# Kernel optimization log

Measured on AMD Instinct MI355X. Metric: run time of the kernel, lower is better.

## Reference

```python
import jax, jax.numpy as jnp
import numpy as np
import math

N = 50000
E = 800000
C_IN = 32
C_H = 256
C_OUT = 3
DEPTH = 3
RATIO = 0.5


def setup_inputs() -> dict:
    key = jax.random.key(0)
    ks = jax.random.split(key, 16)
    s = 0.05  # keep tanh/relu in a healthy range
    f32 = jnp.float32
    return {
        "x": jax.random.normal(ks[0], (N, C_IN), f32),
        "edge_index": jax.random.randint(ks[1], (2, E), 0, N, jnp.int32).astype(jnp.int64),
        "w0_l": jax.random.normal(ks[2], (C_IN, C_H), f32) * s,
        "w0_r": jax.random.normal(ks[3], (C_IN, C_H), f32) * s,
        "b0": jax.random.normal(ks[4], (C_H,), f32) * s,
        "dwl": jax.random.normal(ks[5], (DEPTH, C_H, C_H), f32) * s,
        "dwr": jax.random.normal(ks[6], (DEPTH, C_H, C_H), f32) * s,
        "db": jax.random.normal(ks[7], (DEPTH, C_H), f32) * s,
        "pool_w": jax.random.normal(ks[8], (DEPTH, C_H), f32),
        "uwl": jax.random.normal(ks[9], (DEPTH - 1, C_H, C_H), f32) * s,
        "uwr": jax.random.normal(ks[10], (DEPTH - 1, C_H, C_H), f32) * s,
        "ub": jax.random.normal(ks[11], (DEPTH - 1, C_H), f32) * s,
        "uwl_last": jax.random.normal(ks[12], (C_H, C_OUT), f32) * s,
        "uwr_last": jax.random.normal(ks[13], (C_H, C_OUT), f32) * s,
        "ub_last": jax.random.normal(ks[14], (C_OUT,), f32) * s,
    }


def _sage_max(x, src, dst, n, wl, wr, b):
    # SAGEConv(aggr='max'): out = lin_l(max_j x_j) + lin_r(x_i)
    # dst may contain dummy index n (masked edges); slice it off.
    msg = x[src]                                            # [E, C]
    agg = jax.ops.segment_max(msg, dst, num_segments=n + 1)[:n]
    agg = jnp.where(jnp.isfinite(agg), agg, 0.0)            # empty segments -> 0 (PyG)
    return agg @ wl + b + x @ wr


def _topk_pool(x, src, dst, w, ratio):
    # PyG TopKPooling with min_score=None: score=tanh((x.w)/||w||), keep top-k, rescale.
    n = x.shape[0]
    k = math.ceil(ratio * n)
    score = jnp.tanh((x @ w) / jnp.linalg.norm(w))          # [n]
    vals, perm = jax.lax.top_k(score, k)
    x2 = x[perm] * vals[:, None]
    # relabel edges; dropped edges -> dummy node k (fixed shape, equivalent for max-agg)
    mapping = jnp.full((n + 1,), -1, jnp.int32).at[perm].set(jnp.arange(k, dtype=jnp.int32))
    nsrc, ndst = mapping[src], mapping[dst]
    valid = (nsrc >= 0) & (ndst >= 0)
    src2 = jnp.where(valid, nsrc, 0)
    dst2 = jnp.where(valid, ndst, k)
    return x2, src2, dst2, perm, k


def reference(x, edge_index, w0_l, w0_r, b0, dwl, dwr, db, pool_w,
              uwl, uwr, ub, uwl_last, uwr_last, ub_last):
    n = x.shape[0]
    src = edge_index[0].astype(jnp.int32)
    dst = edge_index[1].astype(jnp.int32)

    x = jax.nn.relu(_sage_max(x, src, dst, n, w0_l, w0_r, b0))
    xs, srcs, dsts, ns, perms = [x], [src], [dst], [n], []

    for i in range(DEPTH):
        x, src, dst, perm, n = _topk_pool(x, src, dst, pool_w[i], RATIO)
        x = jax.nn.relu(_sage_max(x, src, dst, n, dwl[i], dwr[i], db[i]))
        if i < DEPTH - 1:
            xs.append(x); srcs.append(src); dsts.append(dst); ns.append(n)
        perms.append(perm)

    for i in range(DEPTH):
        j = DEPTH - 1 - i
        res, src, dst, n, perm = xs[j], srcs[j], dsts[j], ns[j], perms[j]
        up = jnp.zeros_like(res).at[perm].set(x)
        x = res + up                                         # sum_res=True
        if i < DEPTH - 1:
            x = jax.nn.relu(_sage_max(x, src, dst, n, uwl[i], uwr[i], ub[i]))
        else:
            x = _sage_max(x, src, dst, n, uwl_last, uwr_last, ub_last)

    return jnp.tanh(x) * 0.5
```

## Files before the change

kernel.cpp:

```cpp
#include <hip/hip_runtime.h>
#include <math.h>

#define E_NUM 800000
#define CH 256

typedef __attribute__((ext_vector_type(8))) short short8;
typedef __attribute__((ext_vector_type(4))) float float4v;

__device__ __forceinline__ unsigned f2key(float s) {
  unsigned b = __float_as_uint(s);
  return (b & 0x80000000u) ? ~b : (b | 0x80000000u);
}

__device__ __forceinline__ unsigned pkmax_u16(unsigned a, unsigned b) {
  unsigned d;
  asm("v_pk_max_u16 %0, %1, %2" : "=v"(d) : "v"(a), "v"(b));
  return d;
}


__global__ __launch_bounds__(256) void k_deg(const int* __restrict__ dst, int n,
                                             int* __restrict__ deg) {
  int e = blockIdx.x * 256 + threadIdx.x;
  if (e < E_NUM) { int d = dst[e]; if (d < n) atomicAdd(&deg[d], 1); }
}

__global__ __launch_bounds__(256) void k_scan_block(const int* __restrict__ deg, int n,
                                                    int* __restrict__ incl,
                                                    int* __restrict__ bsum) {
  __shared__ int s[256];
  int i = blockIdx.x * 256 + threadIdx.x;
  int v = (i < n) ? deg[i] : 0;
  s[threadIdx.x] = v;
  __syncthreads();
  for (int o = 1; o < 256; o <<= 1) {
    int t = (threadIdx.x >= o) ? s[threadIdx.x - o] : 0;
    __syncthreads();
    s[threadIdx.x] += t;
    __syncthreads();
  }
  if (i < n) incl[i] = s[threadIdx.x];
  if (threadIdx.x == 255) bsum[blockIdx.x] = s[255];
}

__global__ void k_scan_bsum(int* bsum, int nb, int* total_out) {
  if (threadIdx.x == 0 && blockIdx.x == 0) {
    int acc = 0;
    for (int b = 0; b < nb; b++) { int v = bsum[b]; bsum[b] = acc; acc += v; }
    total_out[0] = acc;
  }
}

__global__ __launch_bounds__(256) void k_scan_final(const int* __restrict__ deg,
                                                    const int* __restrict__ incl,
                                                    const int* __restrict__ bsum, int n,
                                                    int* __restrict__ row,
                                                    int* __restrict__ cursor) {
  int i = blockIdx.x * 256 + threadIdx.x;
  if (i < n) {
    int r = incl[i] - deg[i] + bsum[blockIdx.x];
    row[i] = r;
    cursor[i] = r;
  }
}

__global__ __launch_bounds__(256) void k_fill(const int* __restrict__ src,
                                              const int* __restrict__ dst, int n,
                                              int* __restrict__ cursor,
                                              int* __restrict__ col) {
  int e = blockIdx.x * 256 + threadIdx.x;
  if (e < E_NUM) {
    int d = dst[e];
    if (d < n) { int p = atomicAdd(&cursor[d], 1); col[p] = src[e]; }
  }
}

__global__ __launch_bounds__(256) void k_relabel_deg(const int* __restrict__ srcIn,
                                                     const int* __restrict__ dstIn,
                                                     const int* __restrict__ mapping,
                                                     int kNew, int* __restrict__ srcOut,
                                                     int* __restrict__ dstOut,
                                                     int* __restrict__ deg) {
  int e = blockIdx.x * 256 + threadIdx.x;
  if (e >= E_NUM) return;
  int ns = mapping[srcIn[e]];
  int nd = mapping[dstIn[e]];
  if (ns >= 0 && nd >= 0) {
    srcOut[e] = ns;
    dstOut[e] = nd;
    atomicAdd(&deg[nd], 1);
  } else {
    srcOut[e] = 0;
    dstOut[e] = kNew;
  }
}


__device__ __forceinline__ float4 fmax4(float4 a, float4 b) {
  return make_float4(fmaxf(a.x, b.x), fmaxf(a.y, b.y), fmaxf(a.z, b.z), fmaxf(a.w, b.w));
}

__global__ __launch_bounds__(256) void k_aggmax32(const float* __restrict__ x,
                                                  const int* __restrict__ row,
                                                  const int* __restrict__ col,
                                                  float* __restrict__ out, int n) {
  int node = blockIdx.x * 8 + threadIdx.x / 32;
  int c = threadIdx.x % 32;
  if (node >= n) return;
  int e0 = row[node], e1 = row[node + 1];
  float m0 = -INFINITY, m1 = -INFINITY, m2 = -INFINITY, m3 = -INFINITY;
  int e = e0;
  for (; e + 4 <= e1; e += 4) {
    int s0 = col[e], s1 = col[e + 1], s2 = col[e + 2], s3 = col[e + 3];
    float v0 = x[(size_t)s0 * 32 + c];
    float v1 = x[(size_t)s1 * 32 + c];
    float v2 = x[(size_t)s2 * 32 + c];
    float v3 = x[(size_t)s3 * 32 + c];
    m0 = fmaxf(m0, v0); m1 = fmaxf(m1, v1); m2 = fmaxf(m2, v2); m3 = fmaxf(m3, v3);
  }
  for (; e < e1; e++) m0 = fmaxf(m0, x[(size_t)col[e] * 32 + c]);
  float m = fmaxf(fmaxf(m0, m1), fmaxf(m2, m3));
  out[(size_t)node * 32 + c] = (e1 > e0) ? m : 0.0f;
}

__global__ __launch_bounds__(256) void k_aggmax4(const float* __restrict__ x,
                                                 const int* __restrict__ row,
                                                 const int* __restrict__ col,
                                                 float* __restrict__ out, int n) {
  int lane = threadIdx.x & 63;
  int node = blockIdx.x * 4 + (threadIdx.x >> 6);
  if (node >= n) return;
  int e0 = row[node], e1 = row[node + 1];
  float4 m0 = make_float4(-INFINITY, -INFINITY, -INFINITY, -INFINITY);
  float4 m1 = m0, m2 = m0, m3 = m0;
  int e = e0;
  for (; e + 4 <= e1; e += 4) {
    int s0 = col[e], s1 = col[e + 1], s2 = col[e + 2], s3 = col[e + 3];
    float4 v0 = *(const float4*)&x[(size_t)s0 * CH + lane * 4];
    float4 v1 = *(const float4*)&x[(size_t)s1 * CH + lane * 4];
    float4 v2 = *(const float4*)&x[(size_t)s2 * CH + lane * 4];
    float4 v3 = *(const float4*)&x[(size_t)s3 * CH + lane * 4];
    m0 = fmax4(m0, v0); m1 = fmax4(m1, v1); m2 = fmax4(m2, v2); m3 = fmax4(m3, v3);
  }
  for (; e < e1; e++)
    m0 = fmax4(m0, *(const float4*)&x[(size_t)col[e] * CH + lane * 4]);
  float4 m = fmax4(fmax4(m0, m1), fmax4(m2, m3));
  if (e1 <= e0) m = make_float4(0.f, 0.f, 0.f, 0.f);
  *(float4*)&out[(size_t)node * CH + lane * 4] = m;
}

__device__ __forceinline__ float b2f(unsigned short s) {
  return __uint_as_float(((unsigned)s) << 16);
}

__global__ __launch_bounds__(256) void k_aggmax4_b16(const unsigned short* __restrict__ xb,
                                                     const int* __restrict__ row,
                                                     const int* __restrict__ col,
                                                     float* __restrict__ out, int n) {
  int lane = threadIdx.x & 63;
  int node = blockIdx.x * 4 + (threadIdx.x >> 6);
  if (node >= n) return;
  int e0 = row[node], e1 = row[node + 1];
  uint2 m0 = make_uint2(0u, 0u), m1 = m0, m2 = m0, m3 = m0;
  int e = e0;
  for (; e + 4 <= e1; e += 4) {
    int s0 = col[e], s1 = col[e + 1], s2 = col[e + 2], s3 = col[e + 3];
    uint2 v0 = *(const uint2*)&xb[(size_t)s0 * CH + lane * 4];
    uint2 v1 = *(const uint2*)&xb[(size_t)s1 * CH + lane * 4];
    uint2 v2 = *(const uint2*)&xb[(size_t)s2 * CH + lane * 4];
    uint2 v3 = *(const uint2*)&xb[(size_t)s3 * CH + lane * 4];
    m0.x = pkmax_u16(m0.x, v0.x); m0.y = pkmax_u16(m0.y, v0.y);
    m1.x = pkmax_u16(m1.x, v1.x); m1.y = pkmax_u16(m1.y, v1.y);
    m2.x = pkmax_u16(m2.x, v2.x); m2.y = pkmax_u16(m2.y, v2.y);
    m3.x = pkmax_u16(m3.x, v3.x); m3.y = pkmax_u16(m3.y, v3.y);
  }
  for (; e < e1; e++) {
    uint2 v = *(const uint2*)&xb[(size_t)col[e] * CH + lane * 4];
    m0.x = pkmax_u16(m0.x, v.x);
    m0.y = pkmax_u16(m0.y, v.y);
  }
  m0.x = pkmax_u16(pkmax_u16(m0.x, m1.x), pkmax_u16(m2.x, m3.x));
  m0.y = pkmax_u16(pkmax_u16(m0.y, m1.y), pkmax_u16(m2.y, m3.y));
  float4 m;
  m.x = b2f((unsigned short)(m0.x & 0xFFFFu));
  m.y = b2f((unsigned short)(m0.x >> 16));
  m.z = b2f((unsigned short)(m0.y & 0xFFFFu));
  m.w = b2f((unsigned short)(m0.y >> 16));
  *(float4*)&out[(size_t)node * CH + lane * 4] = m;
}


__global__ __launch_bounds__(256) void k_wprep(const float* __restrict__ src,
                                               unsigned short* __restrict__ dst, int K,
                                               int nmat) {
  int idx = blockIdx.x * 256 + threadIdx.x;
  int total = nmat * K * 256;
  if (idx >= total) return;
  int n = idx % 256;
  int k = (idx / 256) % K;
  int m = idx / (256 * K);
  float v = src[idx];
  unsigned u = __float_as_uint(v);
  unsigned h = u & 0xFFFF0000u;
  float r = v - __uint_as_float(h);
  unsigned short hs = (unsigned short)(h >> 16);
  unsigned short ls = (unsigned short)(__float_as_uint(r) >> 16);
  int ib = k >> 5, kk = k & 31;
  size_t base = (size_t)m * 2 * K * 256;
  size_t o = ((size_t)ib * 256 + n) * 32 + kk;
  dst[base + o] = hs;
  dst[base + (size_t)K * 256 + o] = ls;
}


#define KSTR 40

__global__ __launch_bounds__(256) void k_gemm_mfma(
    const float* __restrict__ A1, const float* __restrict__ A2,
    const unsigned short* __restrict__ W1t, const unsigned short* __restrict__ W2t,
    const float* __restrict__ bias, float* __restrict__ out, int M, int K, int scatter,
    const int* __restrict__ perm, const float* __restrict__ scw,
    float* __restrict__ score, unsigned* __restrict__ hist1) {
  __shared__ unsigned short As_h[64 * KSTR], As_l[64 * KSTR];
  __shared__ float sred[4][64];
  const int t = threadIdx.x;
  const int wave = t >> 6, lane = t & 63;
  const int l15 = lane & 15, qd = lane >> 4;
  const int bm0 = blockIdx.x * 64;
  float4v acc[4][4];
#pragma unroll
  for (int a = 0; a < 4; a++)
#pragma unroll
    for (int b = 0; b < 4; b++) acc[a][b] = (float4v)0.f;
  const int sa_m = t >> 2;
  const int sa_kc = (t & 3) * 8;
  const int rok = (bm0 + sa_m) < M;
  const int nIb = K >> 5;
  for (int ib = 0; ib < 2 * nIb; ib++) {
    const float* A = (ib < nIb) ? A1 : A2;
    const unsigned short* Wt = (ib < nIb) ? W1t : W2t;
    int ib0 = (ib < nIb) ? ib : ib - nIb;
    float va[8];
    {
      const float* ap = &A[(size_t)(bm0 + sa_m) * K + (ib0 << 5) + sa_kc];
      float4 v0 = rok ? *(const float4*)ap : make_float4(0, 0, 0, 0);
      float4 v1 = rok ? *(const float4*)(ap + 4) : make_float4(0, 0, 0, 0);
      va[0] = v0.x; va[1] = v0.y; va[2] = v0.z; va[3] = v0.w;
      va[4] = v1.x; va[5] = v1.y; va[6] = v1.z; va[7] = v1.w;
    }
    short8 bh[4], bl[4];
#pragma unroll
    for (int nt = 0; nt < 4; nt++) {
      size_t rowb = ((size_t)ib0 * 256 + wave * 64 + nt * 16 + l15) * 32 + qd * 8;
      bh[nt] = *(const short8*)&Wt[rowb];
      bl[nt] = *(const short8*)&Wt[(size_t)K * 256 + rowb];
    }
    unsigned hp[4], lp[4];
#pragma unroll
    for (int e = 0; e < 4; e++) {
      unsigned u0 = __float_as_uint(va[2 * e]);
      unsigned u1 = __float_as_uint(va[2 * e + 1]);
      unsigned h0 = u0 & 0xFFFF0000u, h1 = u1 & 0xFFFF0000u;
      float r0 = va[2 * e] - __uint_as_float(h0);
      float r1 = va[2 * e + 1] - __uint_as_float(h1);
      hp[e] = (h0 >> 16) | h1;
      lp[e] = (__float_as_uint(r0) >> 16) | (__float_as_uint(r1) & 0xFFFF0000u);
    }
    __syncthreads();
    *(uint4*)&As_h[sa_m * KSTR + sa_kc] = make_uint4(hp[0], hp[1], hp[2], hp[3]);
    *(uint4*)&As_l[sa_m * KSTR + sa_kc] = make_uint4(lp[0], lp[1], lp[2], lp[3]);
    __syncthreads();
    short8 ah[4], al[4];
#pragma unroll
    for (int mt = 0; mt < 4; mt++) {
      int r = (mt * 16 + l15) * KSTR + qd * 8;
      ah[mt] = *(const short8*)&As_h[r];
      al[mt] = *(const short8*)&As_l[r];
    }
#pragma unroll
    for (int mt = 0; mt < 4; mt++)
#pragma unroll
      for (int nt = 0; nt < 4; nt++) {
        acc[mt][nt] =
            __builtin_amdgcn_mfma_f32_16x16x32_bf16(bh[nt], ah[mt], acc[mt][nt], 0, 0, 0);
        acc[mt][nt] =
            __builtin_amdgcn_mfma_f32_16x16x32_bf16(bl[nt], ah[mt], acc[mt][nt], 0, 0, 0);
        acc[mt][nt] =
            __builtin_amdgcn_mfma_f32_16x16x32_bf16(bh[nt], al[mt], acc[mt][nt], 0, 0, 0);
      }
  }
  const int col0 = wave * 64;
  if (scw) {
    if (t < 64) { sred[0][t] = 0.f; sred[1][t] = 0.f; sred[2][t] = 0.f; sred[3][t] = 0.f; }
    __syncthreads();
  }
  float bias4[4][4], scw4[4][4];
#pragma unroll
  for (int nt = 0; nt < 4; nt++) {
    int cb = col0 + nt * 16 + qd * 4;
    *(float4*)bias4[nt] = *(const float4*)&bias[cb];
    if (scw) *(float4*)scw4[nt] = *(const float4*)&scw[cb];
  }
#pragma unroll
  for (int mt = 0; mt < 4; mt++) {
    int p = bm0 + mt * 16 + l15;
    float sp = 0.f;
    if (p < M) {
      if (scatter) {
        size_t rb = (size_t)perm[p] * CH + col0 + qd * 4;
#pragma unroll
        for (int nt = 0; nt < 4; nt++) {
          float* dp = &out[rb + nt * 16];
          float4 old = *(const float4*)dp;
          float4 v;
          v.x = old.x + fmaxf(acc[mt][nt][0] + bias4[nt][0], 0.f);
          v.y = old.y + fmaxf(acc[mt][nt][1] + bias4[nt][1], 0.f);
          v.z = old.z + fmaxf(acc[mt][nt][2] + bias4[nt][2], 0.f);
          v.w = old.w + fmaxf(acc[mt][nt][3] + bias4[nt][3], 0.f);
          *(float4*)dp = v;
        }
      } else {
        size_t rb = (size_t)p * CH + col0 + qd * 4;
#pragma unroll
        for (int nt = 0; nt < 4; nt++) {
          float4 v;
          v.x = fmaxf(acc[mt][nt][0] + bias4[nt][0], 0.f);
          v.y = fmaxf(acc[mt][nt][1] + bias4[nt][1], 0.f);
          v.z = fmaxf(acc[mt][nt][2] + bias4[nt][2], 0.f);
          v.w = fmaxf(acc[mt][nt][3] + bias4[nt][3], 0.f);
          *(float4*)&out[rb + nt * 16] = v;
          if (scw)
            sp += v.x * scw4[nt][0] + v.y * scw4[nt][1] + v.z * scw4[nt][2] +
                  v.w * scw4[nt][3];
        }
      }
    }
    if (scw) {
      sp += __shfl_xor(sp, 16);
      sp += __shfl_xor(sp, 32);
      if (qd == 0) sred[wave][mt * 16 + l15] = sp;
    }
  }
  if (scw) {
    __syncthreads();
    if (t < 64 && bm0 + t < M) {
      float s = sred[0][t] + sred[1][t] + sred[2][t] + sred[3][t];
      score[bm0 + t] = s;
      atomicAdd(&hist1[f2key(s) >> 16], 1u);
    }
  }
}


__global__ __launch_bounds__(1024) void k_resolve(const unsigned* __restrict__ hist,
                                                  unsigned* __restrict__ state, int pass,
                                                  int k0) {
  __shared__ unsigned csum[1024];
  int t = threadIdx.x;
  int base = 65535 - 64 * t;
  unsigned s = 0;
  for (int j = 0; j < 64; j++) s += hist[base - j];
  csum[t] = s;
  __syncthreads();
  for (int o = 1; o < 1024; o <<= 1) {
    unsigned v = (t >= o) ? csum[t - o] : 0u;
    __syncthreads();
    csum[t] += v;
    __syncthreads();
  }
  unsigned cumBefore = csum[t] - s;
  unsigned kneed = (pass == 0) ? (unsigned)k0 : state[5];
  if (cumBefore < kneed && kneed <= cumBefore + s) {
    unsigned cum = cumBefore;
    for (int j = 0; j < 64; j++) {
      unsigned c = hist[base - j];
      if (cum + c >= kneed) {
        unsigned bucket = (unsigned)(base - j);
        if (pass == 0) {
          state[4] = bucket;
          state[5] = kneed - cum;
        } else {
          state[0] = (state[4] << 16) | bucket;
          state[1] = kneed - cum;
          state[2] = 0u;
          state[3] = 0u;
        }
        break;
      }
      cum += c;
    }
  }
}

__global__ __launch_bounds__(256) void k_hist2(const float* __restrict__ score, int n,
                                               const unsigned* __restrict__ state,
                                               unsigned* __restrict__ hist2) {
  int i = blockIdx.x * 256 + threadIdx.x;
  if (i >= n) return;
  unsigned u = f2key(score[i]);
  if ((u >> 16) == state[4]) atomicAdd(&hist2[u & 0xFFFFu], 1u);
}

__global__ __launch_bounds__(256) void k_compact(const float* __restrict__ score, int n,
                                                 unsigned* __restrict__ state,
                                                 int* __restrict__ perm,
                                                 int* __restrict__ mapping) {
  int i = blockIdx.x * 256 + threadIdx.x;
  if (i > n) return;
  if (i == n) { mapping[n] = -1; return; }
  unsigned Kth = state[0];
  unsigned kneed = state[1];
  unsigned u = f2key(score[i]);
  int m = -1;
  if (u > Kth) {
    unsigned p = atomicAdd(&state[2], 1u);
    perm[p] = i;
    m = (int)p;
  } else if (u == Kth) {
    unsigned tt = atomicAdd(&state[3], 1u);
    if (tt < kneed) {
      unsigned p = atomicAdd(&state[2], 1u);
      perm[p] = i;
      m = (int)p;
    }
  }
  mapping[i] = m;
}

__global__ __launch_bounds__(256) void k_gather(const float* __restrict__ x,
                                                const int* __restrict__ perm,
                                                const float* __restrict__ score,
                                                const float* __restrict__ pw,
                                                float* __restrict__ out, int k) {
  int lane = threadIdx.x & 63;
  int node = blockIdx.x * 4 + (threadIdx.x >> 6);
  float4 w4 = *(const float4*)&pw[lane * 4];
  float nn = w4.x * w4.x + w4.y * w4.y + w4.z * w4.z + w4.w * w4.w;
#pragma unroll
  for (int o = 32; o > 0; o >>= 1) nn += __shfl_down(nn, o);
  nn = __shfl(nn, 0);
  if (node >= k) return;
  int i = perm[node];
  float tv = tanhf(score[i] / sqrtf(nn));
  float4 v = *(const float4*)&x[(size_t)i * CH + lane * 4];
  v.x *= tv; v.y *= tv; v.z *= tv; v.w *= tv;
  *(float4*)&out[(size_t)node * CH + lane * 4] = v;
}


__device__ __forceinline__ unsigned short f2b_rn(float f) {
  unsigned u = __float_as_uint(f);
  u += 0x7FFFu + ((u >> 16) & 1u);
  return (unsigned short)(u >> 16);
}

__global__ __launch_bounds__(256) void k_cvtb16(const float* __restrict__ x,
                                                unsigned short* __restrict__ xb, int n) {
  int lane = threadIdx.x & 63;
  int node = blockIdx.x * 4 + (threadIdx.x >> 6);
  if (node >= n) return;
  float4 a = *(const float4*)&x[(size_t)node * CH + lane * 4];
  ushort4 o;
  o.x = f2b_rn(a.x); o.y = f2b_rn(a.y); o.z = f2b_rn(a.z); o.w = f2b_rn(a.w);
  *(ushort4*)&xb[(size_t)node * CH + lane * 4] = o;
}

__global__ __launch_bounds__(256) void k_final(const unsigned short* __restrict__ XB,
                                               const int* __restrict__ row,
                                               const int* __restrict__ col,
                                               const float* __restrict__ wl,
                                               const float* __restrict__ wr,
                                               const float* __restrict__ b,
                                               float* __restrict__ out, int n) {
  int lane = threadIdx.x & 63;
  int node = blockIdx.x * 4 + (threadIdx.x >> 6);
  if (node >= n) return;
  int e0 = row[node], e1 = row[node + 1];
  uint2 m0 = make_uint2(0u, 0u), m1 = m0, m2 = m0, m3 = m0;
  int e = e0;
  for (; e + 4 <= e1; e += 4) {
    int s0 = col[e], s1 = col[e + 1], s2 = col[e + 2], s3 = col[e + 3];
    uint2 v0 = *(const uint2*)&XB[(size_t)s0 * CH + lane * 4];
    uint2 v1 = *(const uint2*)&XB[(size_t)s1 * CH + lane * 4];
    uint2 v2 = *(const uint2*)&XB[(size_t)s2 * CH + lane * 4];
    uint2 v3 = *(const uint2*)&XB[(size_t)s3 * CH + lane * 4];
    m0.x = pkmax_u16(m0.x, v0.x); m0.y = pkmax_u16(m0.y, v0.y);
    m1.x = pkmax_u16(m1.x, v1.x); m1.y = pkmax_u16(m1.y, v1.y);
    m2.x = pkmax_u16(m2.x, v2.x); m2.y = pkmax_u16(m2.y, v2.y);
    m3.x = pkmax_u16(m3.x, v3.x); m3.y = pkmax_u16(m3.y, v3.y);
  }
  for (; e < e1; e++) {
    uint2 v = *(const uint2*)&XB[(size_t)col[e] * CH + lane * 4];
    m0.x = pkmax_u16(m0.x, v.x);
    m0.y = pkmax_u16(m0.y, v.y);
  }
  m0.x = pkmax_u16(pkmax_u16(m0.x, m1.x), pkmax_u16(m2.x, m3.x));
  m0.y = pkmax_u16(pkmax_u16(m0.y, m1.y), pkmax_u16(m2.y, m3.y));
  float av[4];
  av[0] = b2f((unsigned short)(m0.x & 0xFFFFu));
  av[1] = b2f((unsigned short)(m0.x >> 16));
  av[2] = b2f((unsigned short)(m0.y & 0xFFFFu));
  av[3] = b2f((unsigned short)(m0.y >> 16));
  ushort4 sv4 = *(const ushort4*)&XB[(size_t)node * CH + lane * 4];
  float wlv[12], wrv[12];
  *(float4*)&wlv[0] = ((const float4*)(wl + 12 * lane))[0];
  *(float4*)&wlv[4] = ((const float4*)(wl + 12 * lane))[1];
  *(float4*)&wlv[8] = ((const float4*)(wl + 12 * lane))[2];
  *(float4*)&wrv[0] = ((const float4*)(wr + 12 * lane))[0];
  *(float4*)&wrv[4] = ((const float4*)(wr + 12 * lane))[1];
  *(float4*)&wrv[8] = ((const float4*)(wr + 12 * lane))[2];
  float sv[4] = {b2f(sv4.x), b2f(sv4.y), b2f(sv4.z), b2f(sv4.w)};
  float p[3] = {0.f, 0.f, 0.f};
#pragma unroll
  for (int q = 0; q < 4; q++)
#pragma unroll
    for (int jj = 0; jj < 3; jj++)
      p[jj] += av[q] * wlv[q * 3 + jj] + sv[q] * wrv[q * 3 + jj];
#pragma unroll
  for (int jj = 0; jj < 3; jj++) {
#pragma unroll
    for (int o = 32; o > 0; o >>= 1) p[jj] += __shfl_down(p[jj], o);
  }
  if (lane == 0) {
#pragma unroll
    for (int jj = 0; jj < 3; jj++)
      out[(size_t)node * 3 + jj] = tanhf(p[jj] + b[jj]) * 0.5f;
  }
}


extern "C" void kernel_launch(void* const* d_in, const int* in_sizes, int n_in,
                              void* d_out, int out_size, void* d_ws, size_t ws_size,
                              hipStream_t stream) {
  (void)in_sizes; (void)n_in; (void)out_size; (void)ws_size;
  const float* xin = (const float*)d_in[0];
  const int* ei = (const int*)d_in[1];
  const int* src0 = ei;
  const int* dst0 = ei + E_NUM;
  const float* w0l = (const float*)d_in[2];
  const float* w0r = (const float*)d_in[3];
  const float* b0 = (const float*)d_in[4];
  const float* dwl = (const float*)d_in[5];
  const float* dwr = (const float*)d_in[6];
  const float* db = (const float*)d_in[7];
  const float* poolw = (const float*)d_in[8];
  const float* uwl = (const float*)d_in[9];
  const float* uwr = (const float*)d_in[10];
  const float* ub = (const float*)d_in[11];
  const float* uwlL = (const float*)d_in[12];
  const float* uwrL = (const float*)d_in[13];
  const float* ubL = (const float*)d_in[14];
  float* out = (float*)d_out;

  char* base = (char*)d_ws;
  size_t off = 0;
  auto alloc = [&](size_t bytes) -> void* {
    void* p = base + off;
    off = (off + bytes + 255) & ~(size_t)255;
    return p;
  };

  const int n0 = 50000, n1 = 25000, n2 = 12500, n3 = 6250;
  float* X0 = (float*)alloc((size_t)n0 * CH * 4);
  float* X1 = (float*)alloc((size_t)n1 * CH * 4);
  float* X2 = (float*)alloc((size_t)n2 * CH * 4);
  float* AGG = (float*)alloc((size_t)n1 * CH * 4);
  float* PD = (float*)alloc((size_t)n1 * CH * 4);
  unsigned short* XB = (unsigned short*)alloc((size_t)n0 * CH * 2);
  unsigned short* X1B = (unsigned short*)alloc((size_t)n1 * CH * 2);
  unsigned short* X2B = (unsigned short*)alloc((size_t)n2 * CH * 2);
  int* eA = (int*)alloc((size_t)2 * E_NUM * 4);
  int* eB = (int*)alloc((size_t)2 * E_NUM * 4);
  int* col0 = (int*)alloc((size_t)E_NUM * 4);
  int* col1 = (int*)alloc((size_t)E_NUM * 4);
  int* col2 = (int*)alloc((size_t)E_NUM * 4);
  int* col3 = (int*)alloc((size_t)E_NUM * 4);
  int* row0 = (int*)alloc((size_t)(n0 + 1) * 4);
  int* row1 = (int*)alloc((size_t)(n1 + 1) * 4);
  int* row2 = (int*)alloc((size_t)(n2 + 1) * 4);
  int* row3 = (int*)alloc((size_t)(n3 + 1) * 4);
  int* map1 = (int*)alloc((size_t)(n0 + 1) * 4);
  int* map2 = (int*)alloc((size_t)(n1 + 1) * 4);
  int* map3 = (int*)alloc((size_t)(n2 + 1) * 4);
  int* perm1 = (int*)alloc((size_t)n1 * 4);
  int* perm2 = (int*)alloc((size_t)n2 * 4);
  int* perm3 = (int*)alloc((size_t)n3 * 4);
  float* score = (float*)alloc((size_t)n0 * 4);
  int* deg = (int*)alloc((size_t)n0 * 4);
  int* incl = (int*)alloc((size_t)n0 * 4);
  int* cursor = (int*)alloc((size_t)n0 * 4);
  int* bsum = (int*)alloc((size_t)256 * 4);
  unsigned* state = (unsigned*)alloc(1024);
  unsigned* hist = (unsigned*)alloc((size_t)2 * 65536 * 4);
  const size_t WSZ = (size_t)2 * 256 * 256;
  unsigned short* Wt0l = (unsigned short*)alloc((size_t)2 * 32 * 256 * 2);
  unsigned short* Wt0r = (unsigned short*)alloc((size_t)2 * 32 * 256 * 2);
  unsigned short* Wtdl = (unsigned short*)alloc(3 * WSZ * 2);
  unsigned short* Wtdr = (unsigned short*)alloc(3 * WSZ * 2);
  unsigned short* Wtul = (unsigned short*)alloc(2 * WSZ * 2);
  unsigned short* Wtur = (unsigned short*)alloc(2 * WSZ * 2);

  const int EG = (E_NUM + 255) / 256;

  k_wprep<<<(32 * 256 + 255) / 256, 256, 0, stream>>>(w0l, Wt0l, 32, 1);
  k_wprep<<<(32 * 256 + 255) / 256, 256, 0, stream>>>(w0r, Wt0r, 32, 1);
  k_wprep<<<(3 * 256 * 256 + 255) / 256, 256, 0, stream>>>(dwl, Wtdl, 256, 3);
  k_wprep<<<(3 * 256 * 256 + 255) / 256, 256, 0, stream>>>(dwr, Wtdr, 256, 3);
  k_wprep<<<(2 * 256 * 256 + 255) / 256, 256, 0, stream>>>(uwl, Wtul, 256, 2);
  k_wprep<<<(2 * 256 * 256 + 255) / 256, 256, 0, stream>>>(uwr, Wtur, 256, 2);

  auto csrRest = [&](const int* esrc, const int* edst, int n, int* rowp, int* colp) {
    int nb = (n + 255) / 256;
    k_scan_block<<<nb, 256, 0, stream>>>(deg, n, incl, bsum);
    k_scan_bsum<<<1, 1, 0, stream>>>(bsum, nb, rowp + n);
    k_scan_final<<<nb, 256, 0, stream>>>(deg, incl, bsum, n, rowp, cursor);
    k_fill<<<EG, 256, 0, stream>>>(esrc, edst, n, cursor, colp);
  };

  auto poolLevel = [&](const float* X, const float* pw, int n, int k, int* mapping,
                       int* permL, const int* esrcIn, const int* edstIn, int* esrcOut,
                       int* edstOut, float* Pout) {
    k_resolve<<<1, 1024, 0, stream>>>(hist, state, 0, k);
    k_hist2<<<(n + 255) / 256, 256, 0, stream>>>(score, n, state, hist + 65536);
    k_resolve<<<1, 1024, 0, stream>>>(hist + 65536, state, 1, k);
    k_compact<<<(n + 1 + 255) / 256, 256, 0, stream>>>(score, n, state, permL, mapping);
    k_gather<<<(k + 3) / 4, 256, 0, stream>>>(X, permL, score, pw, Pout, k);
    hipMemsetAsync(deg, 0, (size_t)k * 4, stream);
    k_relabel_deg<<<EG, 256, 0, stream>>>(esrcIn, edstIn, mapping, k, esrcOut, edstOut,
                                          deg);
  };

  auto gemm = [&](const float* A1, const float* A2, const unsigned short* W1t,
                  const unsigned short* W2t, const float* bias, float* o, int M, int K,
                  int scatter, const int* prm, const float* scw, float* sc) {
    if (scw) hipMemsetAsync(hist, 0, (size_t)2 * 65536 * 4, stream);
    k_gemm_mfma<<<(M + 63) / 64, 256, 0, stream>>>(A1, A2, W1t, W2t, bias, o, M, K,
                                                   scatter, prm, scw, sc, hist);
  };

  hipMemsetAsync(deg, 0, (size_t)n0 * 4, stream);
  k_deg<<<EG, 256, 0, stream>>>(dst0, n0, deg);
  csrRest(src0, dst0, n0, row0, col0);
  k_aggmax32<<<(n0 + 7) / 8, 256, 0, stream>>>(xin, row0, col0, AGG, n0);
  gemm(AGG, xin, Wt0l, Wt0r, b0, X0, n0, 32, 0, nullptr, poolw + 0 * CH, score);

  poolLevel(X0, poolw + 0 * CH, n0, n1, map1, perm1, src0, dst0, eA, eA + E_NUM, PD);
  csrRest(eA, eA + E_NUM, n1, row1, col1);
  k_aggmax4<<<(n1 + 3) / 4, 256, 0, stream>>>(PD, row1, col1, AGG, n1);
  gemm(AGG, PD, Wtdl + 0 * WSZ, Wtdr + 0 * WSZ, db + 0 * CH, X1, n1, 256, 0, nullptr,
       poolw + 1 * CH, score);

  poolLevel(X1, poolw + 1 * CH, n1, n2, map2, perm2, eA, eA + E_NUM, eB, eB + E_NUM, PD);
  csrRest(eB, eB + E_NUM, n2, row2, col2);
  k_aggmax4<<<(n2 + 3) / 4, 256, 0, stream>>>(PD, row2, col2, AGG, n2);
  gemm(AGG, PD, Wtdl + 1 * WSZ, Wtdr + 1 * WSZ, db + 1 * CH, X2, n2, 256, 0, nullptr,
       poolw + 2 * CH, score);

  poolLevel(X2, poolw + 2 * CH, n2, n3, map3, perm3, eB, eB + E_NUM, eA, eA + E_NUM, PD);
  csrRest(eA, eA + E_NUM, n3, row3, col3);
  k_aggmax4<<<(n3 + 3) / 4, 256, 0, stream>>>(PD, row3, col3, AGG, n3);
  gemm(AGG, PD, Wtdl + 2 * WSZ, Wtdr + 2 * WSZ, db + 2 * CH, X2, n3, 256, 1, perm3,
       nullptr, nullptr);

  k_cvtb16<<<(n2 + 3) / 4, 256, 0, stream>>>(X2, X2B, n2);
  k_aggmax4_b16<<<(n2 + 3) / 4, 256, 0, stream>>>(X2B, row2, col2, AGG, n2);
  gemm(AGG, X2, Wtul + 0 * WSZ, Wtur + 0 * WSZ, ub + 0 * CH, X1, n2, 256, 1, perm2,
       nullptr, nullptr);

  k_cvtb16<<<(n1 + 3) / 4, 256, 0, stream>>>(X1, X1B, n1);
  k_aggmax4_b16<<<(n1 + 3) / 4, 256, 0, stream>>>(X1B, row1, col1, AGG, n1);
  gemm(AGG, X1, Wtul + 1 * WSZ, Wtur + 1 * WSZ, ub + 1 * CH, X0, n1, 256, 1, perm1,
       nullptr, nullptr);

  k_cvtb16<<<(n0 + 3) / 4, 256, 0, stream>>>(X0, XB, n0);
  k_final<<<(n0 + 3) / 4, 256, 0, stream>>>(XB, row0, col0, uwlL, uwrL, ubL, out, n0);
}
```

Measured before the change: 847.5 us.

## Build pooled CSRs from compacted edge lists and drop third GEMM term on later layers

Removes the relabel kernel that rewrote all 800k edges per pool level. The CSR builder now applies the node mapping on the fly and reads only the surviving edges of the previous level (col plus a new per-edge dst array, counted via row[n]). It also adds a 'terms' parameter to the split-bf16 MFMA GEMM, so the up-path and last down GEMMs skip the A-low product and its LDS store. This cuts edge traffic and MFMA work, at the cost of slightly lower GEMM precision on those layers.

```diff
diff --git a/kernel.cpp b/kernel.cpp
--- a/kernel.cpp
+++ b/kernel.cpp
@@ -19,10 +19,23 @@
 }
 
 
-__global__ __launch_bounds__(256) void k_deg(const int* __restrict__ dst, int n,
-                                             int* __restrict__ deg) {
+__global__ __launch_bounds__(256) void k_deg_map(const int* __restrict__ esrc,
+                                                 const int* __restrict__ edst,
+                                                 const int* __restrict__ ecntPtr,
+                                                 const int* __restrict__ mapping,
+                                                 int* __restrict__ deg) {
   int e = blockIdx.x * 256 + threadIdx.x;
-  if (e < E_NUM) { int d = dst[e]; if (d < n) atomicAdd(&deg[d], 1); }
+  int ne = ecntPtr ? *ecntPtr : E_NUM;
+  if (e >= ne) return;
+  int md;
+  if (mapping) {
+    int ms = mapping[esrc[e]];
+    md = mapping[edst[e]];
+    if (ms < 0 || md < 0) return;
+  } else {
+    md = edst[e];
+  }
+  atomicAdd(&deg[md], 1);
 }
 
 __global__ __launch_bounds__(256) void k_scan_block(const int* __restrict__ deg, int n,
@@ -64,35 +77,28 @@
   }
 }
 
-__global__ __launch_bounds__(256) void k_fill(const int* __restrict__ src,
-                                              const int* __restrict__ dst, int n,
-                                              int* __restrict__ cursor,
-                                              int* __restrict__ col) {
+__global__ __launch_bounds__(256) void k_fill_map(const int* __restrict__ esrc,
+                                                  const int* __restrict__ edst,
+                                                  const int* __restrict__ ecntPtr,
+                                                  const int* __restrict__ mapping,
+                                                  int* __restrict__ cursor,
+                                                  int* __restrict__ col,
+                                                  int* __restrict__ dstv) {
   int e = blockIdx.x * 256 + threadIdx.x;
-  if (e < E_NUM) {
-    int d = dst[e];
-    if (d < n) { int p = atomicAdd(&cursor[d], 1); col[p] = src[e]; }
-  }
-}
-
-__global__ __launch_bounds__(256) void k_relabel_deg(const int* __restrict__ srcIn,
-                                                     const int* __restrict__ dstIn,
-                                                     const int* __restrict__ mapping,
-                                                     int kNew, int* __restrict__ srcOut,
-                                                     int* __restrict__ dstOut,
-                                                     int* __restrict__ deg) {
-  int e = blockIdx.x * 256 + threadIdx.x;
-  if (e >= E_NUM) return;
-  int ns = mapping[srcIn[e]];
-  int nd = mapping[dstIn[e]];
-  if (ns >= 0 && nd >= 0) {
-    srcOut[e] = ns;
-    dstOut[e] = nd;
-    atomicAdd(&deg[nd], 1);
+  int ne = ecntPtr ? *ecntPtr : E_NUM;
+  if (e >= ne) return;
+  int ms, md;
+  if (mapping) {
+    ms = mapping[esrc[e]];
+    md = mapping[edst[e]];
+    if (ms < 0 || md < 0) return;
   } else {
-    srcOut[e] = 0;
-    dstOut[e] = kNew;
-  }
+    ms = esrc[e];
+    md = edst[e];
+  }
+  int p = atomicAdd(&cursor[md], 1);
+  col[p] = ms;
+  if (dstv) dstv[p] = md;
 }
 
 
@@ -220,7 +226,7 @@
     const unsigned short* __restrict__ W1t, const unsigned short* __restrict__ W2t,
     const float* __restrict__ bias, float* __restrict__ out, int M, int K, int scatter,
     const int* __restrict__ perm, const float* __restrict__ scw,
-    float* __restrict__ score, unsigned* __restrict__ hist1) {
+    float* __restrict__ score, unsigned* __restrict__ hist1, int terms) {
   __shared__ unsigned short As_h[64 * KSTR], As_l[64 * KSTR];
   __shared__ float sred[4][64];
   const int t = threadIdx.x;
@@ -268,14 +274,15 @@
     }
     __syncthreads();
     *(uint4*)&As_h[sa_m * KSTR + sa_kc] = make_uint4(hp[0], hp[1], hp[2], hp[3]);
-    *(uint4*)&As_l[sa_m * KSTR + sa_kc] = make_uint4(lp[0], lp[1], lp[2], lp[3]);
+    if (terms == 3)
+      *(uint4*)&As_l[sa_m * KSTR + sa_kc] = make_uint4(lp[0], lp[1], lp[2], lp[3]);
     __syncthreads();
     short8 ah[4], al[4];
 #pragma unroll
     for (int mt = 0; mt < 4; mt++) {
       int r = (mt * 16 + l15) * KSTR + qd * 8;
       ah[mt] = *(const short8*)&As_h[r];
-      al[mt] = *(const short8*)&As_l[r];
+      if (terms == 3) al[mt] = *(const short8*)&As_l[r];
     }
 #pragma unroll
     for (int mt = 0; mt < 4; mt++)
@@ -285,8 +292,9 @@
             __builtin_amdgcn_mfma_f32_16x16x32_bf16(bh[nt], ah[mt], acc[mt][nt], 0, 0, 0);
         acc[mt][nt] =
             __builtin_amdgcn_mfma_f32_16x16x32_bf16(bl[nt], ah[mt], acc[mt][nt], 0, 0, 0);
-        acc[mt][nt] =
-            __builtin_amdgcn_mfma_f32_16x16x32_bf16(bh[nt], al[mt], acc[mt][nt], 0, 0, 0);
+        if (terms == 3)
+          acc[mt][nt] = __builtin_amdgcn_mfma_f32_16x16x32_bf16(bh[nt], al[mt],
+                                                                acc[mt][nt], 0, 0, 0);
       }
   }
   const int col0 = wave * 64;
@@ -569,12 +577,12 @@
   unsigned short* XB = (unsigned short*)alloc((size_t)n0 * CH * 2);
   unsigned short* X1B = (unsigned short*)alloc((size_t)n1 * CH * 2);
   unsigned short* X2B = (unsigned short*)alloc((size_t)n2 * CH * 2);
-  int* eA = (int*)alloc((size_t)2 * E_NUM * 4);
-  int* eB = (int*)alloc((size_t)2 * E_NUM * 4);
   int* col0 = (int*)alloc((size_t)E_NUM * 4);
   int* col1 = (int*)alloc((size_t)E_NUM * 4);
   int* col2 = (int*)alloc((size_t)E_NUM * 4);
   int* col3 = (int*)alloc((size_t)E_NUM * 4);
+  int* dstv1 = (int*)alloc((size_t)E_NUM * 4);
+  int* dstv2 = (int*)alloc((size_t)E_NUM * 4);
   int* row0 = (int*)alloc((size_t)(n0 + 1) * 4);
   int* row1 = (int*)alloc((size_t)(n1 + 1) * 4);
   int* row2 = (int*)alloc((size_t)(n2 + 1) * 4);
@@ -609,68 +617,65 @@
   k_wprep<<<(2 * 256 * 256 + 255) / 256, 256, 0, stream>>>(uwl, Wtul, 256, 2);
   k_wprep<<<(2 * 256 * 256 + 255) / 256, 256, 0, stream>>>(uwr, Wtur, 256, 2);
 
-  auto csrRest = [&](const int* esrc, const int* edst, int n, int* rowp, int* colp) {
+  auto buildCSR = [&](const int* esrc, const int* edst, const int* ecnt,
+                      const int* mapping, int n, int* rowp, int* colp, int* dstvp) {
+    hipMemsetAsync(deg, 0, (size_t)n * 4, stream);
+    k_deg_map<<<EG, 256, 0, stream>>>(esrc, edst, ecnt, mapping, deg);
     int nb = (n + 255) / 256;
     k_scan_block<<<nb, 256, 0, stream>>>(deg, n, incl, bsum);
     k_scan_bsum<<<1, 1, 0, stream>>>(bsum, nb, rowp + n);
     k_scan_final<<<nb, 256, 0, stream>>>(deg, incl, bsum, n, rowp, cursor);
-    k_fill<<<EG, 256, 0, stream>>>(esrc, edst, n, cursor, colp);
+    k_fill_map<<<EG, 256, 0, stream>>>(esrc, edst, ecnt, mapping, cursor, colp, dstvp);
   };
 
   auto poolLevel = [&](const float* X, const float* pw, int n, int k, int* mapping,
-                       int* permL, const int* esrcIn, const int* edstIn, int* esrcOut,
-                       int* edstOut, float* Pout) {
+                       int* permL, float* Pout) {
     k_resolve<<<1, 1024, 0, stream>>>(hist, state, 0, k);
     k_hist2<<<(n + 255) / 256, 256, 0, stream>>>(score, n, state, hist + 65536);
     k_resolve<<<1, 1024, 0, stream>>>(hist + 65536, state, 1, k);
     k_compact<<<(n + 1 + 255) / 256, 256, 0, stream>>>(score, n, state, permL, mapping);
     k_gather<<<(k + 3) / 4, 256, 0, stream>>>(X, permL, score, pw, Pout, k);
-    hipMemsetAsync(deg, 0, (size_t)k * 4, stream);
-    k_relabel_deg<<<EG, 256, 0, stream>>>(esrcIn, edstIn, mapping, k, esrcOut, edstOut,
-                                          deg);
   };
 
   auto gemm = [&](const float* A1, const float* A2, const unsigned short* W1t,
                   const unsigned short* W2t, const float* bias, float* o, int M, int K,
-                  int scatter, const int* prm, const float* scw, float* sc) {
+                  int scatter, const int* prm, const float* scw, float* sc, int terms) {
     if (scw) hipMemsetAsync(hist, 0, (size_t)2 * 65536 * 4, stream);
     k_gemm_mfma<<<(M + 63) / 64, 256, 0, stream>>>(A1, A2, W1t, W2t, bias, o, M, K,
-                                                   scatter, prm, scw, sc, hist);
+                                                   scatter, prm, scw, sc, hist, terms);
   };
 
-  hipMemsetAsync(deg, 0, (size_t)n0 * 4, stream);
-  k_deg<<<EG, 256, 0, stream>>>(dst0, n0, deg);
-  csrRest(src0, dst0, n0, row0, col0);
+  buildCSR(src0, dst0, nullptr, nullptr, n0, row0, col0, nullptr);
   k_aggmax32<<<(n0 + 7) / 8, 256, 0, stream>>>(xin, row0, col0, AGG, n0);
-  gemm(AGG, xin, Wt0l, Wt0r, b0, X0, n0, 32, 0, nullptr, poolw + 0 * CH, score);
-
-  poolLevel(X0, poolw + 0 * CH, n0, n1, map1, perm1, src0, dst0, eA, eA + E_NUM, PD);
-  csrRest(eA, eA + E_NUM, n1, row1, col1);
+  gemm(AGG, xin, Wt0l, Wt0r, b0, X0, n0, 32, 0, nullptr, poolw + 0 * CH, score, 3);
+
+  poolLevel(X0, poolw + 0 * CH, n0, n1, map1, perm1, PD);
+  buildCSR(src0, dst0, nullptr, map1, n1, row1, col1, dstv1);
   k_aggmax4<<<(n1 + 3) / 4, 256, 0, stream>>>(PD, row1, col1, AGG, n1);
   gemm(AGG, PD, Wtdl + 0 * WSZ, Wtdr + 0 * WSZ, db + 0 * CH, X1, n1, 256, 0, nullptr,
-       poolw + 1 * CH, score);
-
-  poolLevel(X1, poolw + 1 * CH, n1, n2, map2, perm2, eA, eA + E_NUM, eB, eB + E_NUM, PD);
-  csrRest(eB, eB + E_NUM, n2, row2, col2);
+       poolw + 1 * CH, score, 3);
+
+  poolLevel(X1, poolw + 1 * CH, n1, n2, map2, perm2, PD);
+  buildCSR(col1, dstv1, row1 + n1, map2, n2, row2, col2, dstv2);
   k_aggmax4<<<(n2 + 3) / 4, 256, 0, stream>>>(PD, row2, col2, AGG, n2);
   gemm(AGG, PD, Wtdl + 1 * WSZ, Wtdr + 1 * WSZ, db + 1 * CH, X2, n2, 256, 0, nullptr,
-       poolw + 2 * CH, score);
-
-  poolLevel(X2, poolw + 2 * CH, n2, n3, map3, perm3, eB, eB + E_NUM, eA, eA + E_NUM, PD);
-  csrRest(eA, eA + E_NUM, n3, row3, col3);
+       poolw + 2 * CH, score, 3);
+
+  poolLevel(X2, poolw + 2 * CH, n2, n3, map3, perm3, PD);
+  buildCSR(col2, dstv2, row2 + n2, map3, n3, row3, col3, nullptr);
   k_aggmax4<<<(n3 + 3) / 4, 256, 0, stream>>>(PD, row3, col3, AGG, n3);
   gemm(AGG, PD, Wtdl + 2 * WSZ, Wtdr + 2 * WSZ, db + 2 * CH, X2, n3, 256, 1, perm3,
-       nullptr, nullptr);
+       nullptr, nullptr, 2);
 
   k_cvtb16<<<(n2 + 3) / 4, 256, 0, stream>>>(X2, X2B, n2);
   k_aggmax4_b16<<<(n2 + 3) / 4, 256, 0, stream>>>(X2B, row2, col2, AGG, n2);
   gemm(AGG, X2, Wtul + 0 * WSZ, Wtur + 0 * WSZ, ub + 0 * CH, X1, n2, 256, 1, perm2,
-       nullptr, nullptr);
+       nullptr, nullptr, 2);
 
   k_cvtb16<<<(n1 + 3) / 4, 256, 0, stream>>>(X1, X1B, n1);
   k_aggmax4_b16<<<(n1 + 3) / 4, 256, 0, stream>>>(X1B, row1, col1, AGG, n1);
   gemm(AGG, X1, Wtul + 1 * WSZ, Wtur + 1 * WSZ, ub + 1 * CH, X0, n1, 256, 1, perm1,
-       nullptr, nullptr);
+       nullptr, nullptr, 2);
 
   k_cvtb16<<<(n0 + 3) / 4, 256, 0, stream>>>(X0, XB, n0);
   k_final<<<(n0 + 3) / 4, 256, 0, stream>>>(XB, row0, col0, uwlL, uwrL, ubL, out, n0);
```

New measurement: 862.6 us. About the same (+1.8%).
